# Performance work log

Measured on AMD Instinct MI355X. Metric: run time of the kernel, lower is better.

The kernel has to match this reference:

```python
import jax, jax.numpy as jnp
import numpy as np

B, L, K, S, D, H, C = 32, 256, 50, 16, 128, 4, 128
V, NN, NU, NS = 50000, 100000, 50000, 5000


def mha(q, k, v, in_w, in_b, out_w, out_b, n_heads):
    # PyTorch nn.MultiheadAttention (batch_first, eval mode) semantics.
    d = q.shape[-1]
    hd = d // n_heads
    wq, wk, wv = jnp.split(in_w, 3, axis=0)
    bq, bk, bv = jnp.split(in_b, 3)
    def heads(t):
        return t.reshape(t.shape[:-1] + (n_heads, hd))
    qh = heads(q @ wq.T + bq)
    kh = heads(k @ wk.T + bk)
    vh = heads(v @ wv.T + bv)
    scores = jnp.einsum('...qhd,...khd->...hqk', qh, kh) / jnp.sqrt(jnp.asarray(hd, q.dtype))
    attn = jax.nn.softmax(scores, axis=-1)
    o = jnp.einsum('...hqk,...khd->...qhd', attn, vh)
    o = o.reshape(o.shape[:-2] + (d,))
    return o @ out_w.T + out_b


def conv1d(x, w, b):
    # x: [B, D, L], w: [Cout, D, k]
    y = jax.lax.conv_general_dilated(x, w, (1,), 'VALID', dimension_numbers=('NCH', 'OIH', 'NCH'))
    return y + b[None, :, None]


def meta_path_module(paths, gru_wih, gru_whh, gru_bih, gru_bhh, in_w, in_b, out_w, out_b, ln_g, ln_b):
    # paths: [B, S, T, D] -> [B, D]
    b, s, t, d = paths.shape
    x = paths.reshape(b * s, t, d)
    def step(h, xt):
        gi = xt @ gru_wih.T + gru_bih
        gh = h @ gru_whh.T + gru_bhh
        ir, iz, inn = jnp.split(gi, 3, axis=-1)
        hr, hz, hn = jnp.split(gh, 3, axis=-1)
        r = jax.nn.sigmoid(ir + hr)
        z = jax.nn.sigmoid(iz + hz)
        n = jnp.tanh(inn + r * hn)
        return (1.0 - z) * n + z * h, None
    h0 = jnp.zeros((b * s, d), paths.dtype)
    h, _ = jax.lax.scan(step, h0, jnp.swapaxes(x, 0, 1))
    enc = h.reshape(b, s, d)
    attn = mha(enc, enc, enc, in_w, in_b, out_w, out_b, H)
    y = enc + attn
    mu = jnp.mean(y, -1, keepdims=True)
    var = jnp.var(y, -1, keepdims=True)
    y = (y - mu) / jnp.sqrt(var + 1e-5) * ln_g + ln_b
    return jnp.mean(y, axis=1)


def _forward(word_table, news_table, user_table, source_table,
             wa_in_w, wa_in_b, wa_out_w, wa_out_b,
             conv_w3, conv_b3, conv_w4, conv_b4, conv_w5, conv_b5, fc_w, fc_b,
             nsn_gru_wih, nsn_gru_whh, nsn_gru_bih, nsn_gru_bhh,
             nsn_in_w, nsn_in_b, nsn_out_w, nsn_out_b, nsn_ln_g, nsn_ln_b,
             nun_gru_wih, nun_gru_whh, nun_gru_bih, nun_gru_bhh,
             nun_in_w, nun_in_b, nun_out_w, nun_out_b, nun_ln_g, nun_ln_b,
             mp_w1, mp_b1, mp_w2, mp_b2, cls_w1, cls_b1, cls_w2, cls_b2,
             news_ids, news_word_indices, word_ctx_ids, nsn_src, nsn_end, nun_usr, nun_end):
    # --- fine-grained word embeds: per-token query attending over context news ---
    base = word_table[news_word_indices]              # [B, L, D]
    ctx = news_table[word_ctx_ids]                    # [B, L, K, D] (dominant gather)
    q = base[:, :, None, :]                           # [B, L, 1, D]
    fine = mha(q, ctx, ctx, wa_in_w, wa_in_b, wa_out_w, wa_out_b, H)[:, :, 0, :]
    pad = (news_word_indices == 0)[..., None]
    doc = jnp.where(pad, jnp.zeros((), base.dtype), fine)   # padding_idx=0 -> zeros
    # --- coarse CNN encoder ---
    x = jnp.swapaxes(doc, 1, 2)                       # [B, D, L]
    pooled = [jnp.max(jax.nn.relu(conv1d(x, w, b)), axis=2)
              for w, b in ((conv_w3, conv_b3), (conv_w4, conv_b4), (conv_w5, conv_b5))]
    semantic = jnp.concatenate(pooled, axis=1) @ fc_w.T + fc_b   # [B, D]
    # --- meta-path interaction ---
    start = jnp.broadcast_to(news_table[news_ids][:, None, :], (B, S, D))
    nsn_paths = jnp.stack([start, source_table[nsn_src], news_table[nsn_end]], axis=2)
    nun_paths = jnp.stack([start, user_table[nun_usr], news_table[nun_end]], axis=2)
    nsn_e = meta_path_module(nsn_paths, nsn_gru_wih, nsn_gru_whh, nsn_gru_bih, nsn_gru_bhh,
                             nsn_in_w, nsn_in_b, nsn_out_w, nsn_out_b, nsn_ln_g, nsn_ln_b)
    nun_e = meta_path_module(nun_paths, nun_gru_wih, nun_gru_whh, nun_gru_bih, nun_gru_bhh,
                             nun_in_w, nun_in_b, nun_out_w, nun_out_b, nun_ln_g, nun_ln_b)
    stack = jnp.stack([nsn_e, nun_e], axis=1)         # [B, 2, D]
    sc = jnp.tanh(stack @ mp_w1.T + mp_b1) @ mp_w2.T + mp_b2
    w = jax.nn.softmax(sc, axis=1)
    struct = jnp.sum(stack * w, axis=1)
    comb = jnp.concatenate([semantic, struct], axis=1)
    hcls = jax.nn.relu(comb @ cls_w1.T + cls_b1)
    return hcls @ cls_w2.T + cls_b2                   # [B, 2]


def setup_inputs() -> dict:
    key = jax.random.key(0)
    ks = iter(jax.random.split(key, 80))
    def p(shape):
        return (jax.random.normal(next(ks), shape, jnp.float32) * 0.02)
    inp = {}
    inp['news_ids'] = jax.random.randint(next(ks), (B,), 0, NN)
    inp['news_word_indices'] = jax.random.randint(next(ks), (B, L), 0, V)
    inp['word_ctx_ids'] = jax.random.randint(next(ks), (B, L, K), 0, NN)
    inp['nsn_src'] = jax.random.randint(next(ks), (B, S), 0, NS)
    inp['nsn_end'] = jax.random.randint(next(ks), (B, S), 0, NN)
    inp['nun_usr'] = jax.random.randint(next(ks), (B, S), 0, NU)
    inp['nun_end'] = jax.random.randint(next(ks), (B, S), 0, NN)
    inp['word_table'] = p((V, D)).at[0].set(0.0)
    inp['news_table'] = p((NN, D))
    inp['user_table'] = p((NU, D))
    inp['source_table'] = p((NS, D))
    inp['wa_in_w'] = p((3 * D, D)); inp['wa_in_b'] = p((3 * D,))
    inp['wa_out_w'] = p((D, D)); inp['wa_out_b'] = p((D,))
    for k in (3, 4, 5):
        inp[f'conv_w{k}'] = p((C, D, k)); inp[f'conv_b{k}'] = p((C,))
    inp['fc_w'] = p((D, 3 * C)); inp['fc_b'] = p((D,))
    for pre in ('nsn', 'nun'):
        inp[f'{pre}_gru_wih'] = p((3 * D, D)); inp[f'{pre}_gru_whh'] = p((3 * D, D))
        inp[f'{pre}_gru_bih'] = p((3 * D,)); inp[f'{pre}_gru_bhh'] = p((3 * D,))
        inp[f'{pre}_in_w'] = p((3 * D, D)); inp[f'{pre}_in_b'] = p((3 * D,))
        inp[f'{pre}_out_w'] = p((D, D)); inp[f'{pre}_out_b'] = p((D,))
        inp[f'{pre}_ln_g'] = jnp.ones((D,), jnp.float32); inp[f'{pre}_ln_b'] = jnp.zeros((D,), jnp.float32)
    inp['mp_w1'] = p((D // 2, D)); inp['mp_b1'] = p((D // 2,))
    inp['mp_w2'] = p((1, D // 2)); inp['mp_b2'] = p((1,))
    inp['cls_w1'] = p((D, 2 * D)); inp['cls_b1'] = p((D,))
    inp['cls_w2'] = p((2, D)); inp['cls_b2'] = p((2,))
    return inp


def reference(word_table, news_table, user_table, source_table,
              wa_in_w, wa_in_b, wa_out_w, wa_out_b,
              conv_w3, conv_b3, conv_w4, conv_b4, conv_w5, conv_b5, fc_w, fc_b,
              nsn_gru_wih, nsn_gru_whh, nsn_gru_bih, nsn_gru_bhh,
              nsn_in_w, nsn_in_b, nsn_out_w, nsn_out_b, nsn_ln_g, nsn_ln_b,
              nun_gru_wih, nun_gru_whh, nun_gru_bih, nun_gru_bhh,
              nun_in_w, nun_in_b, nun_out_w, nun_out_b, nun_ln_g, nun_ln_b,
              mp_w1, mp_b1, mp_w2, mp_b2, cls_w1, cls_b1, cls_w2, cls_b2,
              news_ids, news_word_indices, word_ctx_ids, nsn_src, nsn_end, nun_usr, nun_end):
    return _forward(word_table, news_table, user_table, source_table,
                    wa_in_w, wa_in_b, wa_out_w, wa_out_b,
                    conv_w3, conv_b3, conv_w4, conv_b4, conv_w5, conv_b5, fc_w, fc_b,
                    nsn_gru_wih, nsn_gru_whh, nsn_gru_bih, nsn_gru_bhh,
                    nsn_in_w, nsn_in_b, nsn_out_w, nsn_out_b, nsn_ln_g, nsn_ln_b,
                    nun_gru_wih, nun_gru_whh, nun_gru_bih, nun_gru_bhh,
                    nun_in_w, nun_in_b, nun_out_w, nun_out_b, nun_ln_g, nun_ln_b,
                    mp_w1, mp_b1, mp_w2, mp_b2, cls_w1, cls_b1, cls_w2, cls_b2,
                    news_ids, news_word_indices, word_ctx_ids, nsn_src, nsn_end, nun_usr, nun_end)
```

## Files before the change

### kernel.cpp

```cpp
#include <hip/hip_runtime.h>
#include <hip/hip_bf16.h>

#define BB 32
#define LL 256
#define KC 50
#define SS 16
#define DD 128
#define NH 4
#define CC 128
#define VV 50000
#define NNN 100000
#define NUU 50000
#define NSS 5000

typedef __attribute__((ext_vector_type(8))) short bf16x8;
typedef __attribute__((ext_vector_type(8))) unsigned short u16x8;
typedef __attribute__((ext_vector_type(4))) float f32x4;

#define APAD 132

__device__ __forceinline__ float dot4(float4 a, float4 b){
  return a.x*b.x + a.y*b.y + a.z*b.z + a.w*b.w;
}

__device__ __forceinline__ unsigned short f2bf(float f){
  union { float f; unsigned int u; } v; v.f = f;
  unsigned int r = (v.u + 0x7FFFu + ((v.u >> 16) & 1u)) >> 16;
  return (unsigned short)r;
}
__device__ __forceinline__ float bf2f(unsigned short s){
  union { unsigned int u; float f; } v; v.u = ((unsigned int)s) << 16;
  return v.f;
}

__global__ __launch_bounds__(256) void k_prep(
    const float* __restrict__ w3, const float* __restrict__ w4,
    const float* __restrict__ w5,
    const float* __restrict__ wih0, const float* __restrict__ whh0,
    const float* __restrict__ wih1, const float* __restrict__ whh1,
    const float* __restrict__ in_w, const float* __restrict__ out_w,
    unsigned short* __restrict__ wb3, unsigned short* __restrict__ wb4,
    unsigned short* __restrict__ wb5, unsigned short* __restrict__ wgb,
    unsigned short* __restrict__ wab){
  int e = blockIdx.x*256 + threadIdx.x;
  if (e < CC*DD*3){ int c=e/(DD*3), rm=e%(DD*3), d=rm/3, jj=rm%3;
    wb3[((size_t)jj*CC + c)*DD + d] = f2bf(w3[e]); }
  if (e < CC*DD*4){ int c=e/(DD*4), rm=e%(DD*4), d=rm/4, jj=rm%4;
    wb4[((size_t)jj*CC + c)*DD + d] = f2bf(w4[e]); }
  if (e < CC*DD*5){ int c=e/(DD*5), rm=e%(DD*5), d=rm/5, jj=rm%5;
    wb5[((size_t)jj*CC + c)*DD + d] = f2bf(w5[e]); }
  if (e < 384*DD){
    wgb[e]          = f2bf(wih0[e]);
    wgb[49152 + e]  = f2bf(whh0[e]);
    wgb[98304 + e]  = f2bf(wih1[e]);
    wgb[147456 + e] = f2bf(whh1[e]);
    wab[e]          = f2bf(in_w[e]);
  }
  if (e >= 384*DD && e < 512*DD) wab[e] = f2bf(out_w[e - 384*DD]);
}

__global__ __launch_bounds__(256) void k_projkv(
    const float* __restrict__ news, const unsigned short* __restrict__ wkvb,
    const float* __restrict__ in_b, unsigned short* __restrict__ nK,
    unsigned short* __restrict__ nV){
  __shared__ __align__(16) unsigned short Ts[64*APAD];
  const int tid = threadIdx.x;
  const int r0 = blockIdx.x * 64;
  for (int i = tid; i < 64*32; i += 256){
    int row = i >> 5, j = i & 31;
    int gr = r0 + row;
    float4 v = (gr < NNN) ? ((const float4*)(news + (size_t)gr*DD))[j]
                          : make_float4(0.f,0.f,0.f,0.f);
    unsigned short* d = Ts + row*APAD + j*4;
    d[0]=f2bf(v.x); d[1]=f2bf(v.y); d[2]=f2bf(v.z); d[3]=f2bf(v.w);
  }
  __syncthreads();
  const int wave = tid >> 6;
  const int lane = tid & 63;
  const int l15  = lane & 15;
  const int quad = lane >> 4;
  bf16x8 afr[4][4];
  #pragma unroll
  for (int mt=0; mt<4; mt++)
    #pragma unroll
    for (int ks=0; ks<4; ks++)
      afr[mt][ks] = *(const bf16x8*)(Ts + (mt*16 + l15)*APAD + ks*32 + quad*8);
  __syncthreads();
  for (int pass=0; pass<2; pass++){
    unsigned short* outp = pass ? nV : nK;
    #pragma unroll
    for (int t=0; t<2; t++){
      const int n0 = wave*32 + t*16;
      bf16x8 bfr[4];
      #pragma unroll
      for (int ks=0; ks<4; ks++)
        bfr[ks] = *(const bf16x8*)(wkvb + (size_t)(pass*128 + n0 + l15)*DD + ks*32 + quad*8);
      const float bias = in_b[128 + pass*128 + n0 + l15];
      #pragma unroll
      for (int mt=0; mt<4; mt++){
        f32x4 acc = {0.f,0.f,0.f,0.f};
        #pragma unroll
        for (int ks=0; ks<4; ks++)
          acc = __builtin_amdgcn_mfma_f32_16x16x32_bf16(afr[mt][ks], bfr[ks], acc, 0,0,0);
        const int col = n0 + l15;
        const int rb  = mt*16 + quad*4;
        #pragma unroll
        for (int r=0;r<4;r++)
          Ts[(rb + r)*APAD + col] = f2bf(acc[r] + bias);
      }
    }
    __syncthreads();
    for (int c = tid; c < 64*32; c += 256){
      int row = c >> 5, col4 = (c & 31) * 4;
      int gr = r0 + row;
      if (gr < NNN)
        *(unsigned long long*)(outp + (size_t)gr*128 + col4) =
            *(const unsigned long long*)(Ts + row*APAD + col4);
    }
    __syncthreads();
  }
}

__global__ __launch_bounds__(64) void k_qh(
    const float* __restrict__ word_table, const int* __restrict__ widx,
    const unsigned short* __restrict__ wqb, const float* __restrict__ in_b,
    float* __restrict__ qh){
  const int lane = threadIdx.x;
  const int l15 = lane & 15, quad = lane >> 4;
  const int p0 = blockIdx.x * 16;
  const int row = widx[p0 + l15];
  const float* src = word_table + (size_t)row*DD + quad*8;
  bf16x8 afr[4];
  #pragma unroll
  for (int ks=0; ks<4; ks++){
    float4 v0 = *(const float4*)(src + ks*32);
    float4 v1 = *(const float4*)(src + ks*32 + 4);
    bf16x8 a;
    a[0]=(short)f2bf(v0.x); a[1]=(short)f2bf(v0.y); a[2]=(short)f2bf(v0.z); a[3]=(short)f2bf(v0.w);
    a[4]=(short)f2bf(v1.x); a[5]=(short)f2bf(v1.y); a[6]=(short)f2bf(v1.z); a[7]=(short)f2bf(v1.w);
    afr[ks] = a;
  }
  #pragma unroll
  for (int nt=0; nt<8; nt++){
    const int n0 = nt*16;
    bf16x8 bfr[4];
    #pragma unroll
    for (int ks=0; ks<4; ks++)
      bfr[ks] = *(const bf16x8*)(wqb + (size_t)(n0+l15)*DD + ks*32 + quad*8);
    const float bias = in_b[n0 + l15];
    f32x4 acc = {0.f,0.f,0.f,0.f};
    #pragma unroll
    for (int ks=0; ks<4; ks++)
      acc = __builtin_amdgcn_mfma_f32_16x16x32_bf16(afr[ks], bfr[ks], acc, 0,0,0);
    #pragma unroll
    for (int r=0;r<4;r++){
      int m = quad*4 + r;
      qh[(size_t)(p0+m)*DD + n0 + l15] = acc[r] + bias;
    }
  }
}

__global__ __launch_bounds__(64) void k_attn(
    const float* __restrict__ qh, const unsigned short* __restrict__ nK,
    const unsigned short* __restrict__ nV, const int* __restrict__ ctx_ids,
    unsigned short* __restrict__ o_out){
  const int p = blockIdx.x;
  const int lane = threadIdx.x;
  const int r = lane >> 4;
  const int g = lane & 15;
  const int h = g >> 2;
  __shared__ int ids[52];
  __shared__ float sc[NH][52];
  if (lane < KC) ids[lane] = ctx_ids[(size_t)p*KC + lane];
  float qv[8];
  {
    const float4* qp = (const float4*)(qh + (size_t)p*DD + g*8);
    float4 q0 = qp[0], q1 = qp[1];
    qv[0]=q0.x; qv[1]=q0.y; qv[2]=q0.z; qv[3]=q0.w;
    qv[4]=q1.x; qv[5]=q1.y; qv[6]=q1.z; qv[7]=q1.w;
  }
  __syncthreads();
  for (int kb=0; kb<13; kb++){
    int k2 = kb*4 + r;
    int row = ids[(k2 < KC) ? k2 : 0];
    u16x8 kv = *(const u16x8*)(nK + (size_t)row*DD + g*8);
    float pr = 0.f;
    #pragma unroll
    for (int j=0;j<8;j++) pr += qv[j]*bf2f(kv[j]);
    pr += __shfl_xor(pr, 1, 64);
    pr += __shfl_xor(pr, 2, 64);
    if ((g & 3) == 0 && k2 < KC) sc[h][k2] = pr;
  }
  __syncthreads();
  {
    const int hh = lane >> 4, kc = lane & 15;
    const float scale = 0.17677669529663687f;
    float mx = -1e30f;
    #pragma unroll
    for (int q4=0;q4<4;q4++){ int k2=kc+q4*16; if (k2<KC) mx = fmaxf(mx, sc[hh][k2]); }
    mx = fmaxf(mx, __shfl_xor(mx, 1, 64));
    mx = fmaxf(mx, __shfl_xor(mx, 2, 64));
    mx = fmaxf(mx, __shfl_xor(mx, 4, 64));
    mx = fmaxf(mx, __shfl_xor(mx, 8, 64));
    float sm = 0.f;
    float ev[4];
    #pragma unroll
    for (int q4=0;q4<4;q4++){
      int k2=kc+q4*16;
      ev[q4] = (k2<KC) ? __expf((sc[hh][k2]-mx)*scale) : 0.f;
      sm += ev[q4];
    }
    sm += __shfl_xor(sm, 1, 64);
    sm += __shfl_xor(sm, 2, 64);
    sm += __shfl_xor(sm, 4, 64);
    sm += __shfl_xor(sm, 8, 64);
    float inv = 1.f/sm;
    #pragma unroll
    for (int q4=0;q4<4;q4++){ int k2=kc+q4*16; if (k2<KC) sc[hh][k2] = ev[q4]*inv; }
  }
  __syncthreads();
  float acc[8];
  #pragma unroll
  for (int j=0;j<8;j++) acc[j]=0.f;
  for (int kb=0; kb<13; kb++){
    int k2 = kb*4 + r;
    int row = ids[(k2 < KC) ? k2 : 0];
    float w = (k2 < KC) ? sc[h][k2] : 0.f;
    u16x8 vv = *(const u16x8*)(nV + (size_t)row*DD + g*8);
    #pragma unroll
    for (int j=0;j<8;j++) acc[j] += w*bf2f(vv[j]);
  }
  #pragma unroll
  for (int j=0;j<8;j++){
    acc[j] += __shfl_xor(acc[j], 16, 64);
    acc[j] += __shfl_xor(acc[j], 32, 64);
  }
  if (r == 0){
    u16x8 o;
    #pragma unroll
    for (int j=0;j<8;j++) o[j] = f2bf(acc[j]);
    *(u16x8*)(o_out + (size_t)p*DD + g*8) = o;
  }
}

__global__ __launch_bounds__(64) void k_wo(
    const unsigned short* __restrict__ o_attn, const int* __restrict__ widx,
    const unsigned short* __restrict__ wob, const float* __restrict__ out_b,
    unsigned short* __restrict__ doc){
  const int lane = threadIdx.x;
  const int l15 = lane & 15, quad = lane >> 4;
  const int p0 = blockIdx.x * 16;
  bf16x8 afr[4];
  #pragma unroll
  for (int ks=0; ks<4; ks++)
    afr[ks] = *(const bf16x8*)(o_attn + (size_t)(p0+l15)*DD + ks*32 + quad*8);
  int msk[4];
  #pragma unroll
  for (int r=0;r<4;r++) msk[r] = widx[p0 + quad*4 + r];
  #pragma unroll
  for (int nt=0; nt<8; nt++){
    const int n0 = nt*16;
    bf16x8 bfr[4];
    #pragma unroll
    for (int ks=0; ks<4; ks++)
      bfr[ks] = *(const bf16x8*)(wob + (size_t)(n0+l15)*DD + ks*32 + quad*8);
    const float bias = out_b[n0 + l15];
    f32x4 acc = {0.f,0.f,0.f,0.f};
    #pragma unroll
    for (int ks=0; ks<4; ks++)
      acc = __builtin_amdgcn_mfma_f32_16x16x32_bf16(afr[ks], bfr[ks], acc, 0,0,0);
    #pragma unroll
    for (int r=0;r<4;r++){
      int m = quad*4 + r;
      doc[(size_t)(p0+m)*DD + n0 + l15] = (msk[r] == 0) ? (unsigned short)0
                                                        : f2bf(acc[r] + bias);
    }
  }
}

#define CROWS 68
#define CPAD 136
__global__ __launch_bounds__(256) void k_conv(
    const unsigned short* __restrict__ doc, const unsigned short* __restrict__ wb3,
    const unsigned short* __restrict__ wb4, const unsigned short* __restrict__ wb5,
    float* __restrict__ convp){
  __shared__ __align__(16) char smem[CROWS*CPAD*2];
  unsigned short* ds = (unsigned short*)smem;
  float* smf = (float*)smem;
  const int blk = blockIdx.x;
  const int chunk = blk & 3;
  const int j = (blk >> 2) % 3;
  const int b = blk / 12;
  const int kk = 3 + j;
  const int T = LL - kk + 1;
  const int t0 = chunk * 64;
  const int nrows = 64 + kk - 1;
  const unsigned short* wb = (j==0) ? wb3 : (j==1) ? wb4 : wb5;
  const int tid = threadIdx.x;
  for (int i = tid; i < nrows*16; i += 256){
    int row = i >> 4, q8 = i & 15;
    int gt = t0 + row;
    u16x8 v = (u16x8){0,0,0,0,0,0,0,0};
    if (gt < LL) v = *(const u16x8*)(doc + ((size_t)b*LL + gt)*DD + q8*8);
    *(u16x8*)(ds + row*CPAD + q8*8) = v;
  }
  __syncthreads();
  const int wave = tid >> 6;
  const int lane = tid & 63;
  const int l15  = lane & 15;
  const int quad = lane >> 4;
  f32x4 acc[8];
  #pragma unroll
  for (int nt=0;nt<8;nt++) acc[nt] = (f32x4){0.f,0.f,0.f,0.f};
  for (int jj=0; jj<kk; jj++){
    #pragma unroll
    for (int ks=0; ks<4; ks++){
      bf16x8 af = *(const bf16x8*)(ds + (wave*16 + l15 + jj)*CPAD + ks*32 + quad*8);
      #pragma unroll
      for (int nt=0; nt<8; nt++){
        bf16x8 bf = *(const bf16x8*)(wb + ((size_t)jj*CC + nt*16 + l15)*DD + ks*32 + quad*8);
        acc[nt] = __builtin_amdgcn_mfma_f32_16x16x32_bf16(af, bf, acc[nt], 0,0,0);
      }
    }
  }
  __syncthreads();
  #pragma unroll
  for (int nt=0; nt<8; nt++){
    float mx = -1e30f;
    #pragma unroll
    for (int r=0;r<4;r++){
      int t = t0 + wave*16 + quad*4 + r;
      mx = fmaxf(mx, (t < T) ? acc[nt][r] : -1e30f);
    }
    mx = fmaxf(mx, __shfl_xor(mx, 16, 64));
    mx = fmaxf(mx, __shfl_xor(mx, 32, 64));
    if (quad == 0) smf[wave*128 + nt*16 + l15] = mx;
  }
  __syncthreads();
  if (tid < 128){
    float m4 = fmaxf(fmaxf(smf[tid], smf[128+tid]), fmaxf(smf[256+tid], smf[384+tid]));
    convp[(((size_t)b*3 + j)*4 + chunk)*CC + tid] = m4;
  }
}

#define GSTR 392
__global__ __launch_bounds__(256) void k_gru(
    const float* __restrict__ news_table, const float* __restrict__ user_table,
    const float* __restrict__ source_table,
    const int* __restrict__ news_ids, const int* __restrict__ nsn_src,
    const int* __restrict__ nsn_end, const int* __restrict__ nun_usr,
    const int* __restrict__ nun_end,
    const unsigned short* __restrict__ wgb,
    const float* __restrict__ bih0, const float* __restrict__ bhh0,
    const float* __restrict__ bih1, const float* __restrict__ bhh1,
    float* __restrict__ enc){
  __shared__ __align__(16) unsigned short xs[16][CPAD];
  __shared__ __align__(16) unsigned short hs[16][CPAD];
  __shared__ float hf[8][128];
  __shared__ float gi[8][GSTR];
  __shared__ float gh[8][GSTR];
  const int blk = blockIdx.x;
  const int m  = blk >> 6;
  const int b  = (blk >> 1) & 31;
  const int s0 = (blk & 1) * 8;
  const int tid = threadIdx.x;
  const int wave = tid >> 6, lane = tid & 63, l15 = lane & 15, quad = lane >> 4;
  const unsigned short* Wih = wgb + (size_t)m*2*384*DD;
  const unsigned short* Whh = Wih + 384*DD;
  const float* bih = m ? bih1 : bih0;
  const float* bhh = m ? bhh1 : bhh0;
  for (int i=tid;i<16*CPAD;i+=256){ (&xs[0][0])[i]=0; (&hs[0][0])[i]=0; }
  for (int i=tid;i<8*128;i+=256) (&hf[0][0])[i]=0.f;
  __syncthreads();
  for (int t=0;t<3;t++){
    {
      int s = tid >> 5, j = tid & 31;
      int row; const float* tab;
      if (t==0){ row = news_ids[b]; tab = news_table; }
      else if (t==1){ row = m ? nun_usr[b*SS+s0+s] : nsn_src[b*SS+s0+s];
                      tab = m ? user_table : source_table; }
      else { row = m ? nun_end[b*SS+s0+s] : nsn_end[b*SS+s0+s]; tab = news_table; }
      float4 v = ((const float4*)(tab + (size_t)row*DD))[j];
      unsigned short* dp = &xs[s][j*4];
      dp[0]=f2bf(v.x); dp[1]=f2bf(v.y); dp[2]=f2bf(v.z); dp[3]=f2bf(v.w);
    }
    __syncthreads();
    bf16x8 ax[4], ah[4];
    #pragma unroll
    for (int ks=0;ks<4;ks++){
      ax[ks] = *(const bf16x8*)&xs[l15][ks*32+quad*8];
      ah[ks] = *(const bf16x8*)&hs[l15][ks*32+quad*8];
    }
    #pragma unroll
    for (int nt=0;nt<6;nt++){
      const int n0 = wave*96 + nt*16;
      f32x4 ga = {0.f,0.f,0.f,0.f}, ha = {0.f,0.f,0.f,0.f};
      #pragma unroll
      for (int ks=0;ks<4;ks++){
        bf16x8 bi = *(const bf16x8*)(Wih + (size_t)(n0+l15)*DD + ks*32+quad*8);
        ga = __builtin_amdgcn_mfma_f32_16x16x32_bf16(ax[ks], bi, ga, 0,0,0);
        bf16x8 bh = *(const bf16x8*)(Whh + (size_t)(n0+l15)*DD + ks*32+quad*8);
        ha = __builtin_amdgcn_mfma_f32_16x16x32_bf16(ah[ks], bh, ha, 0,0,0);
      }
      if (quad < 2){
        #pragma unroll
        for (int r=0;r<4;r++){
          gi[quad*4+r][n0+l15] = ga[r];
          gh[quad*4+r][n0+l15] = ha[r];
        }
      }
    }
    __syncthreads();
    #pragma unroll
    for (int k=0;k<4;k++){
      int it = tid + k*256;
      int s = it >> 7, g = it & 127;
      float rr = 1.f/(1.f+__expf(-(gi[s][g] + gh[s][g] + bih[g] + bhh[g])));
      float zz = 1.f/(1.f+__expf(-(gi[s][128+g] + gh[s][128+g] + bih[128+g] + bhh[128+g])));
      float nn = tanhf(gi[s][256+g] + bih[256+g] + rr*(gh[s][256+g] + bhh[256+g]));
      float hnew = (1.f-zz)*nn + zz*hf[s][g];
      hf[s][g] = hnew;
      hs[s][g] = f2bf(hnew);
    }
    __syncthreads();
  }
  {
    int s = tid >> 5, j = tid & 31;
    float4 v = ((const float4*)hf[s])[j];
    ((float4*)(enc + (((size_t)m*BB + b)*SS + (s0+s))*DD))[j] = v;
  }
}

__global__ __launch_bounds__(128, 2) void k_metamha(
    const float* __restrict__ enc,
    const float* __restrict__ inw0, const float* __restrict__ inb0,
    const float* __restrict__ outw0, const float* __restrict__ outb0,
    const float* __restrict__ lng0, const float* __restrict__ lnb0,
    const float* __restrict__ inw1, const float* __restrict__ inb1,
    const float* __restrict__ outw1, const float* __restrict__ outb1,
    const float* __restrict__ lng1, const float* __restrict__ lnb1,
    float* __restrict__ meta_e){
  const int m = blockIdx.x >> 5;
  const int b = blockIdx.x & 31;
  const int c = threadIdx.x;
  const float* in_w  = m?inw1:inw0;  const float* in_b  = m?inb1:inb0;
  const float* out_w = m?outw1:outw0; const float* out_b = m?outb1:outb0;
  const float* lng   = m?lng1:lng0;  const float* lnb   = m?lnb1:lnb0;
  __shared__ float e[16][128], q[16][128], k[16][128], v[16][128];
  __shared__ float at[4][16][16];
  __shared__ float mu[16], rs[16];
  const float* esrc = enc + ((size_t)m*BB + b)*SS*DD;
  for (int i=c;i<16*128;i+=128) ((float*)e)[i] = esrc[i];
  __syncthreads();
  {
    float aq[16], ak[16], av[16];
    float bq = in_b[c], bk = in_b[128+c], bv = in_b[256+c];
    #pragma unroll
    for (int s=0;s<16;s++){ aq[s]=bq; ak[s]=bk; av[s]=bv; }
    const float4* wq4 = (const float4*)(in_w + c*DD);
    const float4* wk4 = (const float4*)(in_w + (128+c)*DD);
    const float4* wv4 = (const float4*)(in_w + (256+c)*DD);
    for (int j=0;j<32;j++){
      float4 a0=wq4[j], a1=wk4[j], a2=wv4[j];
      #pragma unroll
      for (int s=0;s<16;s++){
        float4 ev = ((const float4*)e[s])[j];
        aq[s]+=dot4(a0,ev); ak[s]+=dot4(a1,ev); av[s]+=dot4(a2,ev);
      }
    }
    #pragma unroll
    for (int s=0;s<16;s++){ q[s][c]=aq[s]; k[s][c]=ak[s]; v[s][c]=av[s]; }
  }
  __syncthreads();
  for (int r=0;r<8;r++){
    int lin = r*128 + c;
    int h = lin >> 8, qi = (lin>>4)&15, ki = lin&15;
    float sum=0.f;
    const float* qp = &q[qi][h*32];
    const float* kp = &k[ki][h*32];
    for (int x=0;x<32;x++) sum += qp[x]*kp[x];
    at[h][qi][ki] = sum * 0.17677669529663687f;
  }
  __syncthreads();
  if (c < 64){
    int h = c>>4, qi = c&15;
    float mx=-1e30f;
    for (int ki=0;ki<16;ki++) mx = fmaxf(mx, at[h][qi][ki]);
    float sm=0.f;
    for (int ki=0;ki<16;ki++){ float ee=__expf(at[h][qi][ki]-mx); at[h][qi][ki]=ee; sm+=ee; }
    float inv=1.f/sm;
    for (int ki=0;ki<16;ki++) at[h][qi][ki]*=inv;
  }
  __syncthreads();
  {
    int h = c>>5;
    float o[16];
    #pragma unroll
    for (int s=0;s<16;s++){
      float acc=0.f;
      for (int ki=0;ki<16;ki++) acc += at[h][s][ki]*v[ki][c];
      o[s]=acc;
    }
    __syncthreads();
    #pragma unroll
    for (int s=0;s<16;s++) q[s][c]=o[s];
  }
  __syncthreads();
  {
    float ay[16];
    float bo = out_b[c];
    #pragma unroll
    for (int s=0;s<16;s++) ay[s] = bo + e[s][c];
    const float4* wo4 = (const float4*)(out_w + c*DD);
    for (int j=0;j<32;j++){
      float4 wv_ = wo4[j];
      #pragma unroll
      for (int s=0;s<16;s++) ay[s] += dot4(wv_, ((const float4*)q[s])[j]);
    }
    __syncthreads();
    #pragma unroll
    for (int s=0;s<16;s++) e[s][c] = ay[s];
  }
  __syncthreads();
  if (c < 16){
    float sm=0.f;
    for (int d=0;d<128;d++) sm += e[c][d];
    float mean = sm*(1.f/128.f);
    float vs=0.f;
    for (int d=0;d<128;d++){ float df = e[c][d]-mean; vs += df*df; }
    mu[c]=mean; rs[c]=rsqrtf(vs*(1.f/128.f) + 1e-5f);
  }
  __syncthreads();
  {
    float g = lng[c], bb2 = lnb[c];
    float acc=0.f;
    #pragma unroll
    for (int s=0;s<16;s++) acc += (e[s][c]-mu[s])*rs[s]*g + bb2;
    meta_e[((size_t)m*BB+b)*DD + c] = acc * (1.f/16.f);
  }
}

__global__ __launch_bounds__(128) void k_final(
    const float* __restrict__ convp,
    const float* __restrict__ cb3, const float* __restrict__ cb4,
    const float* __restrict__ cb5,
    const float* __restrict__ fc_w, const float* __restrict__ fc_b,
    const float* __restrict__ meta_e,
    const float* __restrict__ mp_w1, const float* __restrict__ mp_b1,
    const float* __restrict__ mp_w2, const float* __restrict__ mp_b2,
    const float* __restrict__ cls_w1, const float* __restrict__ cls_b1,
    const float* __restrict__ cls_w2, const float* __restrict__ cls_b2,
    float* __restrict__ out){
  const int b = blockIdx.x;
  const int c = threadIdx.x;
  __shared__ float pooled[384];
  __shared__ float comb[256];
  __shared__ float hcls[128];
  __shared__ float tt[2][64];
  __shared__ float wsc[2];
  for (int idx=c; idx<384; idx+=128){
    int j = idx >> 7, cc2 = idx & 127;
    const float* base = convp + (((size_t)b*3 + j)*4)*CC + cc2;
    float mx = -1e30f;
    for (int ci=0;ci<4;ci++) mx = fmaxf(mx, base[ci*CC]);
    const float* cb = (j==0)?cb3:(j==1)?cb4:cb5;
    pooled[idx] = fmaxf(mx + cb[cc2], 0.f);
  }
  __syncthreads();
  {
    float acc = fc_b[c];
    const float* wr = fc_w + (size_t)c*384;
    for (int i=0;i<384;i++) acc += pooled[i]*wr[i];
    comb[c] = acc;
  }
  if (c < 64){
    for (int m=0;m<2;m++){
      const float* ev = meta_e + ((size_t)m*BB+b)*DD;
      float acc = mp_b1[c];
      const float* wr = mp_w1 + (size_t)c*DD;
      for (int i=0;i<DD;i++) acc += ev[i]*wr[i];
      tt[m][c] = tanhf(acc);
    }
  }
  __syncthreads();
  if (c == 0){
    float s0 = mp_b2[0], s1 = mp_b2[0];
    for (int j=0;j<64;j++){ s0 += tt[0][j]*mp_w2[j]; s1 += tt[1][j]*mp_w2[j]; }
    float mx = fmaxf(s0,s1);
    float e0 = __expf(s0-mx), e1 = __expf(s1-mx);
    wsc[0] = e0/(e0+e1); wsc[1] = e1/(e0+e1);
  }
  __syncthreads();
  comb[128+c] = wsc[0]*meta_e[((size_t)b)*DD + c]
              + wsc[1]*meta_e[((size_t)(BB+b))*DD + c];
  __syncthreads();
  {
    float acc = cls_b1[c];
    const float* wr = cls_w1 + (size_t)c*256;
    for (int i=0;i<256;i++) acc += comb[i]*wr[i];
    hcls[c] = fmaxf(acc, 0.f);
  }
  __syncthreads();
  if (c < 2){
    float acc = cls_b2[c];
    const float* wr = cls_w2 + (size_t)c*DD;
    for (int i=0;i<DD;i++) acc += hcls[i]*wr[i];
    out[b*2 + c] = acc;
  }
}

extern "C" void kernel_launch(void* const* d_in, const int* in_sizes, int n_in,
                              void* d_out, int out_size, void* d_ws, size_t ws_size,
                              hipStream_t stream){
  const int* news_ids = (const int*)d_in[0];
  const int* nwi      = (const int*)d_in[1];
  const int* ctx_ids  = (const int*)d_in[2];
  const int* nsn_src  = (const int*)d_in[3];
  const int* nsn_end  = (const int*)d_in[4];
  const int* nun_usr  = (const int*)d_in[5];
  const int* nun_end  = (const int*)d_in[6];
  const float* word_table   = (const float*)d_in[7];
  const float* news_table   = (const float*)d_in[8];
  const float* user_table   = (const float*)d_in[9];
  const float* source_table = (const float*)d_in[10];
  const float* wa_in_w  = (const float*)d_in[11];
  const float* wa_in_b  = (const float*)d_in[12];
  const float* wa_out_w = (const float*)d_in[13];
  const float* wa_out_b = (const float*)d_in[14];
  const float* conv_w3 = (const float*)d_in[15];
  const float* conv_b3 = (const float*)d_in[16];
  const float* conv_w4 = (const float*)d_in[17];
  const float* conv_b4 = (const float*)d_in[18];
  const float* conv_w5 = (const float*)d_in[19];
  const float* conv_b5 = (const float*)d_in[20];
  const float* fc_w = (const float*)d_in[21];
  const float* fc_b = (const float*)d_in[22];
  const float* wih0 = (const float*)d_in[23];
  const float* whh0 = (const float*)d_in[24];
  const float* bih0 = (const float*)d_in[25];
  const float* bhh0 = (const float*)d_in[26];
  const float* inw0 = (const float*)d_in[27];
  const float* inb0 = (const float*)d_in[28];
  const float* outw0 = (const float*)d_in[29];
  const float* outb0 = (const float*)d_in[30];
  const float* lng0 = (const float*)d_in[31];
  const float* lnb0 = (const float*)d_in[32];
  const float* wih1 = (const float*)d_in[33];
  const float* whh1 = (const float*)d_in[34];
  const float* bih1 = (const float*)d_in[35];
  const float* bhh1 = (const float*)d_in[36];
  const float* inw1 = (const float*)d_in[37];
  const float* inb1 = (const float*)d_in[38];
  const float* outw1 = (const float*)d_in[39];
  const float* outb1 = (const float*)d_in[40];
  const float* lng1 = (const float*)d_in[41];
  const float* lnb1 = (const float*)d_in[42];
  const float* mp_w1 = (const float*)d_in[43];
  const float* mp_b1 = (const float*)d_in[44];
  const float* mp_w2 = (const float*)d_in[45];
  const float* mp_b2 = (const float*)d_in[46];
  const float* cls_w1 = (const float*)d_in[47];
  const float* cls_b1 = (const float*)d_in[48];
  const float* cls_w2 = (const float*)d_in[49];
  const float* cls_b2 = (const float*)d_in[50];

  char* wsb = (char*)d_ws;
  unsigned short* nK = (unsigned short*)wsb;
  unsigned short* nV = nK + (size_t)NNN*DD;
  unsigned short* wb3 = nV + (size_t)NNN*DD;
  unsigned short* wb4 = wb3 + (size_t)CC*DD*3;
  unsigned short* wb5 = wb4 + (size_t)CC*DD*4;
  unsigned short* wgb = wb5 + (size_t)CC*DD*5;
  unsigned short* wab = wgb + (size_t)4*384*DD;
  float* qh     = (float*)(wab + (size_t)512*DD);
  unsigned short* o_at = (unsigned short*)(qh + (size_t)BB*LL*DD);
  unsigned short* doc  = (unsigned short*)((float*)o_at + (size_t)BB*LL*DD);
  float* convp  = (float*)doc + (size_t)BB*LL*DD;
  float* enc    = convp + BB*3*4*CC;
  float* meta_e = enc + (size_t)2*BB*SS*DD;
  const size_t need_bytes = (size_t)((char*)(meta_e + 2*BB*DD) - wsb);
  if (ws_size < need_bytes) return;

  const unsigned short* wqb  = wab;
  const unsigned short* wkvb = wab + (size_t)128*DD;
  const unsigned short* wob  = wab + (size_t)384*DD;

  k_prep<<<dim3(320), dim3(256), 0, stream>>>(conv_w3, conv_w4, conv_w5,
      wih0, whh0, wih1, whh1, wa_in_w, wa_out_w, wb3, wb4, wb5, wgb, wab);
  k_projkv<<<dim3((NNN+63)/64), dim3(256), 0, stream>>>(news_table, wkvb, wa_in_b, nK, nV);
  k_qh<<<dim3(BB*LL/16), dim3(64), 0, stream>>>(word_table, nwi, wqb, wa_in_b, qh);
  k_attn<<<dim3(BB*LL), dim3(64), 0, stream>>>(qh, nK, nV, ctx_ids, o_at);
  k_wo<<<dim3(BB*LL/16), dim3(64), 0, stream>>>(o_at, nwi, wob, wa_out_b, doc);
  k_conv<<<dim3(BB*3*4), dim3(256), 0, stream>>>(doc, wb3, wb4, wb5, convp);
  k_gru<<<dim3(128), dim3(256), 0, stream>>>(news_table, user_table, source_table,
      news_ids, nsn_src, nsn_end, nun_usr, nun_end,
      wgb, bih0, bhh0, bih1, bhh1, enc);
  k_metamha<<<dim3(64), dim3(128), 0, stream>>>(enc,
      inw0, inb0, outw0, outb0, lng0, lnb0,
      inw1, inb1, outw1, outb1, lng1, lnb1, meta_e);
  k_final<<<dim3(BB), dim3(128), 0, stream>>>(convp, conv_b3, conv_b4, conv_b5,
      fc_w, fc_b, meta_e, mp_w1, mp_b1, mp_w2, mp_b2,
      cls_w1, cls_b1, cls_w2, cls_b2, (float*)d_out);
}
```

Before: 391.2 us.

## Rewrite meta-path MHA kernel with bf16 MFMA projections and 256 threads

The meta-path attention kernel now runs its QKV input projection, QK^T scores and output projection on bf16 MFMA instructions instead of scalar fp32 dot products. The MHA weights are pre-converted to bf16 in the prep kernel. The block grows to four waves, and the LayerNorm statistics use a shuffle reduction across 16 lanes in place of a serial loop over 16 threads. This removes a long serial fp32 kernel from the tail of the pipeline, at the cost of bf16 rounding in the attention path and extra conversion work in the prep kernel.

```diff
diff --git a/kernel.cpp b/kernel.cpp
--- a/kernel.cpp
+++ b/kernel.cpp
@@ -39,9 +39,11 @@
     const float* __restrict__ wih0, const float* __restrict__ whh0,
     const float* __restrict__ wih1, const float* __restrict__ whh1,
     const float* __restrict__ in_w, const float* __restrict__ out_w,
+    const float* __restrict__ inw0, const float* __restrict__ outw0,
+    const float* __restrict__ inw1, const float* __restrict__ outw1,
     unsigned short* __restrict__ wb3, unsigned short* __restrict__ wb4,
     unsigned short* __restrict__ wb5, unsigned short* __restrict__ wgb,
-    unsigned short* __restrict__ wab){
+    unsigned short* __restrict__ wab, unsigned short* __restrict__ wmh){
   int e = blockIdx.x*256 + threadIdx.x;
   if (e < CC*DD*3){ int c=e/(DD*3), rm=e%(DD*3), d=rm/3, jj=rm%3;
     wb3[((size_t)jj*CC + c)*DD + d] = f2bf(w3[e]); }
@@ -57,6 +59,12 @@
     wab[e]          = f2bf(in_w[e]);
   }
   if (e >= 384*DD && e < 512*DD) wab[e] = f2bf(out_w[e - 384*DD]);
+  if (e < 512*DD){
+    float s0 = (e < 384*DD) ? inw0[e] : outw0[e - 384*DD];
+    float s1 = (e < 384*DD) ? inw1[e] : outw1[e - 384*DD];
+    wmh[e]                 = f2bf(s0);
+    wmh[(size_t)512*DD + e] = f2bf(s1);
+  }
 }
 
 __global__ __launch_bounds__(256) void k_projkv(
@@ -431,113 +439,162 @@
   }
 }
 
-__global__ __launch_bounds__(128, 2) void k_metamha(
+#define MPAD 136
+__global__ __launch_bounds__(256) void k_metamha(
     const float* __restrict__ enc,
-    const float* __restrict__ inw0, const float* __restrict__ inb0,
-    const float* __restrict__ outw0, const float* __restrict__ outb0,
+    const unsigned short* __restrict__ wmh,
+    const float* __restrict__ inb0, const float* __restrict__ outb0,
     const float* __restrict__ lng0, const float* __restrict__ lnb0,
-    const float* __restrict__ inw1, const float* __restrict__ inb1,
-    const float* __restrict__ outw1, const float* __restrict__ outb1,
+    const float* __restrict__ inb1, const float* __restrict__ outb1,
     const float* __restrict__ lng1, const float* __restrict__ lnb1,
     float* __restrict__ meta_e){
   const int m = blockIdx.x >> 5;
   const int b = blockIdx.x & 31;
-  const int c = threadIdx.x;
-  const float* in_w  = m?inw1:inw0;  const float* in_b  = m?inb1:inb0;
-  const float* out_w = m?outw1:outw0; const float* out_b = m?outb1:outb0;
-  const float* lng   = m?lng1:lng0;  const float* lnb   = m?lnb1:lnb0;
-  __shared__ float e[16][128], q[16][128], k[16][128], v[16][128];
-  __shared__ float at[4][16][16];
+  const int tid = threadIdx.x;
+  const int wave = tid >> 6, lane = tid & 63, l15 = lane & 15, quad = lane >> 4;
+  const unsigned short* W = wmh + (size_t)m*512*DD;
+  const float* in_b  = m ? inb1 : inb0;
+  const float* out_b = m ? outb1 : outb0;
+  const float* lng   = m ? lng1 : lng0;
+  const float* lnb   = m ? lnb1 : lnb0;
+
+  __shared__ __align__(16) unsigned short ebf[16][MPAD];
+  __shared__ __align__(16) unsigned short qb[16][MPAD];
+  __shared__ __align__(16) unsigned short kb[16][MPAD];
+  __shared__ __align__(16) unsigned short ob[16][MPAD];
+  __shared__ float vf[16][128];
+  __shared__ float er[16][132];
+  __shared__ float at[NH][16][16];
   __shared__ float mu[16], rs[16];
+  __shared__ float part[2][128];
+
   const float* esrc = enc + ((size_t)m*BB + b)*SS*DD;
-  for (int i=c;i<16*128;i+=128) ((float*)e)[i] = esrc[i];
-  __syncthreads();
-  {
-    float aq[16], ak[16], av[16];
-    float bq = in_b[c], bk = in_b[128+c], bv = in_b[256+c];
-    #pragma unroll
-    for (int s=0;s<16;s++){ aq[s]=bq; ak[s]=bk; av[s]=bv; }
-    const float4* wq4 = (const float4*)(in_w + c*DD);
-    const float4* wk4 = (const float4*)(in_w + (128+c)*DD);
-    const float4* wv4 = (const float4*)(in_w + (256+c)*DD);
-    for (int j=0;j<32;j++){
-      float4 a0=wq4[j], a1=wk4[j], a2=wv4[j];
-      #pragma unroll
-      for (int s=0;s<16;s++){
-        float4 ev = ((const float4*)e[s])[j];
-        aq[s]+=dot4(a0,ev); ak[s]+=dot4(a1,ev); av[s]+=dot4(a2,ev);
+  for (int i = tid; i < 16*32; i += 256){
+    int s = i >> 5, j = i & 31;
+    float4 v = ((const float4*)esrc)[i];
+    ((float4*)er[s])[j] = v;
+    unsigned short* dp = &ebf[s][j*4];
+    dp[0]=f2bf(v.x); dp[1]=f2bf(v.y); dp[2]=f2bf(v.z); dp[3]=f2bf(v.w);
+  }
+  __syncthreads();
+  {
+    bf16x8 ax[4];
+    #pragma unroll
+    for (int ks=0;ks<4;ks++) ax[ks] = *(const bf16x8*)&ebf[l15][ks*32+quad*8];
+    #pragma unroll
+    for (int nt=0; nt<6; nt++){
+      const int n0 = wave*96 + nt*16;
+      f32x4 acc = {0.f,0.f,0.f,0.f};
+      #pragma unroll
+      for (int ks=0;ks<4;ks++){
+        bf16x8 bw = *(const bf16x8*)(W + (size_t)(n0+l15)*DD + ks*32+quad*8);
+        acc = __builtin_amdgcn_mfma_f32_16x16x32_bf16(ax[ks], bw, acc, 0,0,0);
       }
-    }
-    #pragma unroll
-    for (int s=0;s<16;s++){ q[s][c]=aq[s]; k[s][c]=ak[s]; v[s][c]=av[s]; }
-  }
-  __syncthreads();
-  for (int r=0;r<8;r++){
-    int lin = r*128 + c;
-    int h = lin >> 8, qi = (lin>>4)&15, ki = lin&15;
-    float sum=0.f;
-    const float* qp = &q[qi][h*32];
-    const float* kp = &k[ki][h*32];
-    for (int x=0;x<32;x++) sum += qp[x]*kp[x];
-    at[h][qi][ki] = sum * 0.17677669529663687f;
-  }
-  __syncthreads();
-  if (c < 64){
-    int h = c>>4, qi = c&15;
+      const float bias = in_b[n0+l15];
+      const int col = n0 + l15;
+      #pragma unroll
+      for (int r=0;r<4;r++){
+        int row = quad*4+r;
+        float val = acc[r] + bias;
+        if (n0 < 128)      qb[row][col]       = f2bf(val);
+        else if (n0 < 256) kb[row][col-128]   = f2bf(val);
+        else               vf[row][col-256]   = val;
+      }
+    }
+  }
+  __syncthreads();
+  {
+    const int h = wave;
+    bf16x8 aq = *(const bf16x8*)&qb[l15][h*32 + quad*8];
+    bf16x8 ak = *(const bf16x8*)&kb[l15][h*32 + quad*8];
+    f32x4 z = {0.f,0.f,0.f,0.f};
+    f32x4 acc = __builtin_amdgcn_mfma_f32_16x16x32_bf16(aq, ak, z, 0,0,0);
+    #pragma unroll
+    for (int r=0;r<4;r++)
+      at[h][quad*4+r][l15] = acc[r] * 0.17677669529663687f;
+  }
+  __syncthreads();
+  if (tid < 64){
+    int h = tid>>4, qi = tid&15;
     float mx=-1e30f;
+    #pragma unroll
     for (int ki=0;ki<16;ki++) mx = fmaxf(mx, at[h][qi][ki]);
     float sm=0.f;
-    for (int ki=0;ki<16;ki++){ float ee=__expf(at[h][qi][ki]-mx); at[h][qi][ki]=ee; sm+=ee; }
+    float ee[16];
+    #pragma unroll
+    for (int ki=0;ki<16;ki++){ ee[ki]=__expf(at[h][qi][ki]-mx); sm+=ee[ki]; }
     float inv=1.f/sm;
-    for (int ki=0;ki<16;ki++) at[h][qi][ki]*=inv;
-  }
-  __syncthreads();
-  {
-    int h = c>>5;
-    float o[16];
-    #pragma unroll
-    for (int s=0;s<16;s++){
+    #pragma unroll
+    for (int ki=0;ki<16;ki++) at[h][qi][ki]=ee[ki]*inv;
+  }
+  __syncthreads();
+  {
+    int c = tid & 127, h = c >> 5;
+    int sBase = (tid >> 7) * 8;
+    #pragma unroll
+    for (int s=0;s<8;s++){
       float acc=0.f;
-      for (int ki=0;ki<16;ki++) acc += at[h][s][ki]*v[ki][c];
-      o[s]=acc;
-    }
-    __syncthreads();
-    #pragma unroll
-    for (int s=0;s<16;s++) q[s][c]=o[s];
-  }
-  __syncthreads();
-  {
-    float ay[16];
-    float bo = out_b[c];
-    #pragma unroll
-    for (int s=0;s<16;s++) ay[s] = bo + e[s][c];
-    const float4* wo4 = (const float4*)(out_w + c*DD);
-    for (int j=0;j<32;j++){
-      float4 wv_ = wo4[j];
-      #pragma unroll
-      for (int s=0;s<16;s++) ay[s] += dot4(wv_, ((const float4*)q[s])[j]);
-    }
-    __syncthreads();
-    #pragma unroll
-    for (int s=0;s<16;s++) e[s][c] = ay[s];
-  }
-  __syncthreads();
-  if (c < 16){
-    float sm=0.f;
-    for (int d=0;d<128;d++) sm += e[c][d];
-    float mean = sm*(1.f/128.f);
-    float vs=0.f;
-    for (int d=0;d<128;d++){ float df = e[c][d]-mean; vs += df*df; }
-    mu[c]=mean; rs[c]=rsqrtf(vs*(1.f/128.f) + 1e-5f);
-  }
-  __syncthreads();
-  {
+      #pragma unroll
+      for (int ki=0;ki<16;ki++) acc += at[h][sBase+s][ki]*vf[ki][c];
+      ob[sBase+s][c] = f2bf(acc);
+    }
+  }
+  __syncthreads();
+  {
+    bf16x8 ao[4];
+    #pragma unroll
+    for (int ks=0;ks<4;ks++) ao[ks] = *(const bf16x8*)&ob[l15][ks*32+quad*8];
+    #pragma unroll
+    for (int nt=0; nt<2; nt++){
+      const int n0 = wave*32 + nt*16;
+      f32x4 acc = {0.f,0.f,0.f,0.f};
+      #pragma unroll
+      for (int ks=0;ks<4;ks++){
+        bf16x8 bw = *(const bf16x8*)(W + (size_t)(384 + n0+l15)*DD + ks*32+quad*8);
+        acc = __builtin_amdgcn_mfma_f32_16x16x32_bf16(ao[ks], bw, acc, 0,0,0);
+      }
+      const float bias = out_b[n0+l15];
+      const int col = n0 + l15;
+      #pragma unroll
+      for (int r=0;r<4;r++){
+        int row = quad*4 + r;
+        er[row][col] += acc[r] + bias;
+      }
+    }
+  }
+  __syncthreads();
+  {
+    int row = tid >> 4, i = tid & 15;
+    const float* yr = &er[row][i*8];
+    float s1=0.f, s2=0.f;
+    #pragma unroll
+    for (int j2=0;j2<8;j2++){ float y=yr[j2]; s1+=y; s2+=y*y; }
+    #pragma unroll
+    for (int msk=1; msk<16; msk<<=1){
+      s1 += __shfl_xor(s1, msk, 64);
+      s2 += __shfl_xor(s2, msk, 64);
+    }
+    if (i==0){
+      float mean = s1*(1.f/128.f);
+      mu[row]=mean;
+      rs[row]=rsqrtf(s2*(1.f/128.f) - mean*mean + 1e-5f);
+    }
+  }
+  __syncthreads();
+  {
+    int c = tid & 127, half = tid >> 7;
     float g = lng[c], bb2 = lnb[c];
     float acc=0.f;
     #pragma unroll
-    for (int s=0;s<16;s++) acc += (e[s][c]-mu[s])*rs[s]*g + bb2;
-    meta_e[((size_t)m*BB+b)*DD + c] = acc * (1.f/16.f);
-  }
+    for (int s=0;s<8;s++){
+      int ss = half*8+s;
+      acc += (er[ss][c]-mu[ss])*rs[ss]*g + bb2;
+    }
+    part[half][c]=acc;
+  }
+  __syncthreads();
+  if (tid < 128)
+    meta_e[((size_t)m*BB+b)*DD + tid] = (part[0][tid]+part[1][tid]) * (1.f/16.f);
 }
 
 __global__ __launch_bounds__(128) void k_final(
@@ -672,7 +729,8 @@
   unsigned short* wb5 = wb4 + (size_t)CC*DD*4;
   unsigned short* wgb = wb5 + (size_t)CC*DD*5;
   unsigned short* wab = wgb + (size_t)4*384*DD;
-  float* qh     = (float*)(wab + (size_t)512*DD);
+  unsigned short* wmh = wab + (size_t)512*DD;
+  float* qh     = (float*)(wmh + (size_t)2*512*DD);
   unsigned short* o_at = (unsigned short*)(qh + (size_t)BB*LL*DD);
   unsigned short* doc  = (unsigned short*)((float*)o_at + (size_t)BB*LL*DD);
   float* convp  = (float*)doc + (size_t)BB*LL*DD;
@@ -686,7 +744,9 @@
   const unsigned short* wob  = wab + (size_t)384*DD;
 
   k_prep<<<dim3(320), dim3(256), 0, stream>>>(conv_w3, conv_w4, conv_w5,
-      wih0, whh0, wih1, whh1, wa_in_w, wa_out_w, wb3, wb4, wb5, wgb, wab);
+      wih0, whh0, wih1, whh1, wa_in_w, wa_out_w,
+      inw0, outw0, inw1, outw1,
+      wb3, wb4, wb5, wgb, wab, wmh);
   k_projkv<<<dim3((NNN+63)/64), dim3(256), 0, stream>>>(news_table, wkvb, wa_in_b, nK, nV);
   k_qh<<<dim3(BB*LL/16), dim3(64), 0, stream>>>(word_table, nwi, wqb, wa_in_b, qh);
   k_attn<<<dim3(BB*LL), dim3(64), 0, stream>>>(qh, nK, nV, ctx_ids, o_at);
@@ -695,9 +755,9 @@
   k_gru<<<dim3(128), dim3(256), 0, stream>>>(news_table, user_table, source_table,
       news_ids, nsn_src, nsn_end, nun_usr, nun_end,
       wgb, bih0, bhh0, bih1, bhh1, enc);
-  k_metamha<<<dim3(64), dim3(128), 0, stream>>>(enc,
-      inw0, inb0, outw0, outb0, lng0, lnb0,
-      inw1, inb1, outw1, outb1, lng1, lnb1, meta_e);
+  k_metamha<<<dim3(64), dim3(256), 0, stream>>>(enc, wmh,
+      inb0, outb0, lng0, lnb0,
+      inb1, outb1, lng1, lnb1, meta_e);
   k_final<<<dim3(BB), dim3(128), 0, stream>>>(convp, conv_b3, conv_b4, conv_b5,
       fc_w, fc_b, meta_e, mp_w1, mp_b1, mp_w2, mp_b2,
       cls_w1, cls_b1, cls_w2, cls_b2, (float*)d_out);
```

Result: faster. 362.5 us (-7.3%).
